# Kernel optimization log

Measured on AMD Instinct MI355X. Metric: run time of the kernel, lower is better.

Reference implementation:

```python
import jax, jax.numpy as jnp
import numpy as np

DT = 0.1
TAU_HP = 12.3  # Tm1 high-pass time constant
TAU_LP = 2.3   # Tm1 low-pass time constant

N_NEURONS = 200_000
N_EDGES = 6_400_000
N_TM1 = 25_000
STEPS = 50


def setup_inputs() -> dict:
    key = jax.random.key(0)
    k1, k2, k3, k4 = jax.random.split(key, 4)
    tm1_input = jax.random.normal(k1, (STEPS, N_TM1), dtype=jnp.float32)
    weights = jax.random.normal(k2, (N_EDGES,), dtype=jnp.float32) * 0.1
    tau = jnp.ones((N_NEURONS,), dtype=jnp.float32)      # tau_init = 1.0 per type
    vrest = jnp.zeros((N_NEURONS,), dtype=jnp.float32)   # vrest_init = 0.0 per type
    source_idx = jax.random.randint(k3, (N_EDGES,), 0, N_NEURONS, dtype=jnp.int32)
    target_idx = jax.random.randint(k4, (N_EDGES,), 0, N_NEURONS, dtype=jnp.int32)
    return {
        "tm1_input": tm1_input,
        "weights": weights,
        "tau": tau,
        "vrest": vrest,
        "source_idx": source_idx,
        "target_idx": target_idx,
        "n_tm1": N_TM1,
    }


def reference(tm1_input, weights, tau, vrest, source_idx, target_idx, n_tm1):
    n_neurons = tau.shape[0]

    def step(carry, x):
        v, tm1_f, tm1_v = carry
        # Tm1 temporal filters: high-pass then rectify then low-pass
        hp_out = x - tm1_f                                   # [n_tm1]
        tm1_f_new = tm1_f + DT * (x - tm1_f) / TAU_HP
        rect_out = jax.nn.relu(hp_out)
        # write (old) tm1_v into the Tm1 slice of v before recurrence
        v = v.at[:n_tm1].set(tm1_v)
        tm1_v_new = tm1_v + DT * (rect_out - tm1_v) / TAU_LP
        # gather -> weight -> scatter-add message passing
        r = jax.nn.relu(v)                                   # [n_neurons]
        edge_currents = r[source_idx] * weights              # [n_edges]
        synaptic_input = jax.ops.segment_sum(
            edge_currents, target_idx, num_segments=n_neurons)
        external = jnp.zeros_like(v).at[:n_tm1].set(tm1_v_new)
        dv = (-v + synaptic_input + vrest + external) / tau
        dv = dv.at[:n_tm1].set(0.0)                          # Tm1 driven by its filters
        v = v + DT * dv
        return (v, tm1_f_new, tm1_v_new), None

    v0 = jnp.zeros((tau.shape[0],), dtype=tm1_input.dtype)
    f0 = jnp.zeros((n_tm1,), dtype=tm1_input.dtype)
    tv0 = jnp.zeros((n_tm1,), dtype=tm1_input.dtype)
    (v, _, _), _ = jax.lax.scan(step, (v0, f0, tv0), tm1_input)
    return v[None, :]  # [1, n_neurons], matches torch batch=1
```

## Files before the change

### kernel.cpp

```cpp
#include <hip/hip_runtime.h>
#include <hip/hip_bf16.h>

#define DT 0.1f
#define TAU_HP 12.3f
#define TAU_LP 2.3f
#define SCAN_B 1024

#define BSHIFT 7
#define BMASK 127
#define BMAX 2048
#define CHUNK 16384
#define B4_CAP 6144


__global__ void init_kernel(float* __restrict__ v,
                            float* __restrict__ tm1_f,
                            float* __restrict__ tm1_v,
                            int n_neurons, int n_tm1) {
    int i = blockIdx.x * blockDim.x + threadIdx.x;
    if (i < n_neurons) v[i] = 0.0f;
    if (i < n_tm1) { tm1_f[i] = 0.0f; tm1_v[i] = 0.0f; }
}

__global__ void bhist_kernel(const int* __restrict__ tgt, int* __restrict__ blkhist,
                             int n_edges, int nb, int nblk) {
    __shared__ int hist[BMAX];
    int b = blockIdx.x;
    for (int i = threadIdx.x; i < nb; i += blockDim.x) hist[i] = 0;
    __syncthreads();
    int base = b * CHUNK;
    int end = min(base + CHUNK, n_edges);
    for (int k = base + threadIdx.x; k < end; k += blockDim.x)
        atomicAdd(&hist[tgt[k] >> BSHIFT], 1);
    __syncthreads();
    for (int i = threadIdx.x; i < nb; i += blockDim.x)
        blkhist[(size_t)i * nblk + b] = hist[i];
}

__global__ void scan1_kernel(const int* in, int* out, int* bsums, int n) {
    __shared__ int s[SCAN_B];
    int gid = blockIdx.x * SCAN_B + threadIdx.x;
    int x = (gid < n) ? in[gid] : 0;
    s[threadIdx.x] = x;
    __syncthreads();
    for (int off = 1; off < SCAN_B; off <<= 1) {
        int t = (threadIdx.x >= off) ? s[threadIdx.x - off] : 0;
        __syncthreads();
        s[threadIdx.x] += t;
        __syncthreads();
    }
    if (gid < n) out[gid] = s[threadIdx.x] - x;
    if (threadIdx.x == SCAN_B - 1) bsums[blockIdx.x] = s[SCAN_B - 1];
}

__global__ void scan2_kernel(int* bsums, int nb) {
    __shared__ int s[SCAN_B];
    int x = (threadIdx.x < nb) ? bsums[threadIdx.x] : 0;
    s[threadIdx.x] = x;
    __syncthreads();
    for (int off = 1; off < SCAN_B; off <<= 1) {
        int t = (threadIdx.x >= off) ? s[threadIdx.x - off] : 0;
        __syncthreads();
        s[threadIdx.x] += t;
        __syncthreads();
    }
    if (threadIdx.x < nb) bsums[threadIdx.x] = s[threadIdx.x] - x;
}

__global__ void scanadd_kernel(int* data, const int* __restrict__ bsums, int n) {
    int gid = blockIdx.x * blockDim.x + threadIdx.x;
    if (gid < n) data[gid] += bsums[gid / SCAN_B];
}

__global__ void bin_kernel(const int* __restrict__ src, const int* __restrict__ tgt,
                           const float* __restrict__ w, const int* __restrict__ scanned,
                           int2* __restrict__ edges, int n_edges, int nb, int nblk) {
    __shared__ int cur[BMAX];
    int b = blockIdx.x;
    for (int i = threadIdx.x; i < nb; i += blockDim.x)
        cur[i] = scanned[(size_t)i * nblk + b];
    __syncthreads();
    int base = b * CHUNK;
    int end = min(base + CHUNK, n_edges);
    for (int k = base + threadIdx.x; k < end; k += blockDim.x) {
        int t = tgt[k];
        int pos = atomicAdd(&cur[t >> BSHIFT], 1);
        edges[pos] = make_int2(src[k] | ((t & BMASK) << 18), __float_as_int(w[k]));
    }
}

__global__ void finalize_kernel(int2* edges, const int* __restrict__ scanned,
                                int* __restrict__ row_start,
                                int n_neurons, int n_edges, int nb, int nblk) {
    __shared__ int2 buf[B4_CAP];
    __shared__ int hist[BMASK + 1], ls[BMASK + 1], cur[BMASK + 1];
    int b = blockIdx.x;
    int beg = scanned[(size_t)b * nblk];
    int end = (b == nb - 1) ? n_edges : scanned[(size_t)(b + 1) * nblk];
    int n = min(end - beg, B4_CAP);

    for (int k = threadIdx.x; k < n; k += blockDim.x) buf[k] = edges[beg + k];
    if (threadIdx.x <= BMASK) hist[threadIdx.x] = 0;
    __syncthreads();
    for (int k = threadIdx.x; k < n; k += blockDim.x)
        atomicAdd(&hist[(buf[k].x >> 18) & BMASK], 1);
    __syncthreads();
    if (threadIdx.x <= BMASK) ls[threadIdx.x] = hist[threadIdx.x];
    __syncthreads();
    for (int off = 1; off <= BMASK; off <<= 1) {
        int t = (threadIdx.x <= BMASK && threadIdx.x >= off) ? ls[threadIdx.x - off] : 0;
        __syncthreads();
        if (threadIdx.x <= BMASK) ls[threadIdx.x] += t;
        __syncthreads();
    }
    if (threadIdx.x <= BMASK) {
        int excl = ls[threadIdx.x] - hist[threadIdx.x];
        cur[threadIdx.x] = excl;
        int t = (b << BSHIFT) + threadIdx.x;
        if (t < n_neurons) row_start[t] = beg + excl;
    }
    if (b == nb - 1 && threadIdx.x == 0) row_start[n_neurons] = n_edges;
    __syncthreads();
    for (int k = threadIdx.x; k < n; k += blockDim.x) {
        int2 r = buf[k];
        int pos = atomicAdd(&cur[(r.x >> 18) & BMASK], 1);
        edges[beg + pos] = make_int2(r.x & 0x3FFFF, r.y);
    }
}


__global__ void neuron_kernel(float* __restrict__ v,
                              const float* __restrict__ syn,
                              float* __restrict__ tm1_f,
                              float* __restrict__ tm1_v,
                              const float* __restrict__ x,
                              const float* __restrict__ tau,
                              const float* __restrict__ vrest,
                              int n_neurons, int n_tm1, int do_update) {
    int i = blockIdx.x * blockDim.x + threadIdx.x;
    if (i >= n_neurons) return;

    if (i < n_tm1) {
        float f  = tm1_f[i];
        float tv = tm1_v[i];
        float xi = x[i];
        float hp = xi - f;
        tm1_f[i] = f + DT * (xi - f) / TAU_HP;
        v[i] = tv;
        float rect = fmaxf(hp, 0.0f);
        tm1_v[i] = tv + DT * (rect - tv) / TAU_LP;
    } else if (do_update) {
        float vi = v[i];
        float dv = (-vi + syn[i] + vrest[i]) / tau[i];
        v[i] = vi + DT * dv;
    }
}

__global__ void gather_kernel(const int* __restrict__ row_start,
                              const int2* __restrict__ edges,
                              const float* __restrict__ v,
                              float* __restrict__ syn, int n) {
    int tid  = blockIdx.x * blockDim.x + threadIdx.x;
    int row  = tid >> 4;
    int lane = tid & 15;
    if (row >= n) return;
    int s = row_start[row];
    int e = row_start[row + 1];
    float sum = 0.0f;
    for (int p = (s & ~1) + 2 * lane; p < e; p += 32) {
        int4 q = *(const int4*)(edges + p);
        if (p >= s)     sum += fmaxf(v[q.x], 0.0f) * __int_as_float(q.y);
        if (p + 1 < e)  sum += fmaxf(v[q.z], 0.0f) * __int_as_float(q.w);
    }
    sum += __shfl_xor(sum, 8);
    sum += __shfl_xor(sum, 4);
    sum += __shfl_xor(sum, 2);
    sum += __shfl_xor(sum, 1);
    if (lane == 0) syn[row] = sum;
}

__global__ void final_kernel(const float* __restrict__ v,
                             const float* __restrict__ syn,
                             const float* __restrict__ tau,
                             const float* __restrict__ vrest,
                             float* __restrict__ out,
                             int n_neurons, int n_tm1) {
    int i = blockIdx.x * blockDim.x + threadIdx.x;
    if (i >= n_neurons) return;
    float vi = v[i];
    if (i >= n_tm1) {
        vi = vi + DT * ((-vi + syn[i] + vrest[i]) / tau[i]);
    }
    out[i] = vi;
}

extern "C" void kernel_launch(void* const* d_in, const int* in_sizes, int n_in,
                              void* d_out, int out_size, void* d_ws, size_t ws_size,
                              hipStream_t stream) {
    const float* tm1_input  = (const float*)d_in[0];
    const float* weights    = (const float*)d_in[1];
    const float* tau        = (const float*)d_in[2];
    const float* vrest      = (const float*)d_in[3];
    const int*   source_idx = (const int*)d_in[4];
    const int*   target_idx = (const int*)d_in[5];

    const int n_edges   = in_sizes[1];
    const int n_neurons = in_sizes[2];
    const int n_tm1     = 25000;
    const int steps     = in_sizes[0] / n_tm1;

    const int nb   = (n_neurons + BMASK) >> BSHIFT;
    const int nblk = (n_edges + CHUNK - 1) / CHUNK;
    const int n_scan = nb * nblk;

    size_t off = 0;
    auto alloc = [&](size_t n) { size_t o = off; off += n; return o; };
    int* ws_i = (int*)d_ws;
    float* ws_f = (float*)d_ws;

    int2*  edges     = (int2*)(ws_i + alloc((size_t)(n_edges + 2) * 2));
    float* v         = ws_f + alloc(n_neurons);
    float* syn       = ws_f + alloc(n_neurons);
    float* tm1_f     = ws_f + alloc(n_tm1);
    float* tm1_v     = ws_f + alloc(n_tm1);
    int*   row_start = ws_i + alloc(n_neurons + 1);
    int*   blkhist   = ws_i + alloc((size_t)n_scan);
    int*   bsums     = ws_i + alloc(SCAN_B);
    (void)ws_size;

    float* out = (float*)d_out;

    const int B = 256;
    const int gridN = (n_neurons + B - 1) / B;
    const int gridG = ((n_neurons * 16) + B - 1) / B;
    const int nScanBlocks = (n_scan + SCAN_B - 1) / SCAN_B;
    const int gridSA = (n_scan + B - 1) / B;

    init_kernel<<<gridN, B, 0, stream>>>(v, tm1_f, tm1_v, n_neurons, n_tm1);
    bhist_kernel<<<nblk, 1024, 0, stream>>>(target_idx, blkhist, n_edges, nb, nblk);
    scan1_kernel<<<nScanBlocks, SCAN_B, 0, stream>>>(blkhist, blkhist, bsums, n_scan);
    scan2_kernel<<<1, SCAN_B, 0, stream>>>(bsums, nScanBlocks);
    scanadd_kernel<<<gridSA, B, 0, stream>>>(blkhist, bsums, n_scan);
    bin_kernel<<<nblk, 1024, 0, stream>>>(source_idx, target_idx, weights, blkhist,
                                          edges, n_edges, nb, nblk);
    finalize_kernel<<<nb, 1024, 0, stream>>>(edges, blkhist, row_start,
                                             n_neurons, n_edges, nb, nblk);

    for (int t = 0; t < steps; ++t) {
        neuron_kernel<<<gridN, B, 0, stream>>>(
            v, syn, tm1_f, tm1_v,
            tm1_input + (size_t)t * n_tm1,
            tau, vrest, n_neurons, n_tm1, t > 0 ? 1 : 0);
        gather_kernel<<<gridG, B, 0, stream>>>(row_start, edges, v, syn, n_neurons);
    }

    final_kernel<<<gridN, B, 0, stream>>>(v, syn, tau, vrest, out, n_neurons, n_tm1);
}
```

Baseline: 2.149 ms.

## Fuse neuron update into gather with ping-pong state and drop Tm1-target edges

Merges the per-step neuron update and the synaptic gather into one step kernel that reads the previous state buffer and writes the next, double-buffering v. This removes the separate update kernel, the syn array round trip and the final kernel. Edges whose target is a Tm1 neuron are dropped while the CSR is built, since their synaptic input is overwritten anyway, which shrinks the per-step gather. The Tm1 low-pass state is now carried in v itself, and the binning chunk size is doubled. The risk is in the restructured Tm1 recurrence and last-step handling, which must still match the reference.

```diff
diff --git a/kernel.cpp b/kernel.cpp
--- a/kernel.cpp
+++ b/kernel.cpp
@@ -9,29 +9,30 @@
 #define BSHIFT 7
 #define BMASK 127
 #define BMAX 2048
-#define CHUNK 16384
+#define CHUNK 32768
 #define B4_CAP 6144
 
 
-__global__ void init_kernel(float* __restrict__ v,
+__global__ void init_kernel(float* __restrict__ vA,
                             float* __restrict__ tm1_f,
-                            float* __restrict__ tm1_v,
                             int n_neurons, int n_tm1) {
     int i = blockIdx.x * blockDim.x + threadIdx.x;
-    if (i < n_neurons) v[i] = 0.0f;
-    if (i < n_tm1) { tm1_f[i] = 0.0f; tm1_v[i] = 0.0f; }
+    if (i < n_neurons) vA[i] = 0.0f;
+    if (i < n_tm1) tm1_f[i] = 0.0f;
 }
 
 __global__ void bhist_kernel(const int* __restrict__ tgt, int* __restrict__ blkhist,
-                             int n_edges, int nb, int nblk) {
+                             int n_edges, int n_tm1, int nb, int nblk) {
     __shared__ int hist[BMAX];
     int b = blockIdx.x;
     for (int i = threadIdx.x; i < nb; i += blockDim.x) hist[i] = 0;
     __syncthreads();
     int base = b * CHUNK;
     int end = min(base + CHUNK, n_edges);
-    for (int k = base + threadIdx.x; k < end; k += blockDim.x)
-        atomicAdd(&hist[tgt[k] >> BSHIFT], 1);
+    for (int k = base + threadIdx.x; k < end; k += blockDim.x) {
+        int t = tgt[k];
+        if (t >= n_tm1) atomicAdd(&hist[t >> BSHIFT], 1);
+    }
     __syncthreads();
     for (int i = threadIdx.x; i < nb; i += blockDim.x)
         blkhist[(size_t)i * nblk + b] = hist[i];
@@ -53,7 +54,7 @@
     if (threadIdx.x == SCAN_B - 1) bsums[blockIdx.x] = s[SCAN_B - 1];
 }
 
-__global__ void scan2_kernel(int* bsums, int nb) {
+__global__ void scan2_kernel(int* bsums, int nb, int* total) {
     __shared__ int s[SCAN_B];
     int x = (threadIdx.x < nb) ? bsums[threadIdx.x] : 0;
     s[threadIdx.x] = x;
@@ -64,6 +65,7 @@
         s[threadIdx.x] += t;
         __syncthreads();
     }
+    if (threadIdx.x == nb - 1) *total = s[threadIdx.x];
     if (threadIdx.x < nb) bsums[threadIdx.x] = s[threadIdx.x] - x;
 }
 
@@ -74,7 +76,8 @@
 
 __global__ void bin_kernel(const int* __restrict__ src, const int* __restrict__ tgt,
                            const float* __restrict__ w, const int* __restrict__ scanned,
-                           int2* __restrict__ edges, int n_edges, int nb, int nblk) {
+                           int2* __restrict__ edges, int n_edges, int n_tm1,
+                           int nb, int nblk) {
     __shared__ int cur[BMAX];
     int b = blockIdx.x;
     for (int i = threadIdx.x; i < nb; i += blockDim.x)
@@ -84,6 +87,7 @@
     int end = min(base + CHUNK, n_edges);
     for (int k = base + threadIdx.x; k < end; k += blockDim.x) {
         int t = tgt[k];
+        if (t < n_tm1) continue;
         int pos = atomicAdd(&cur[t >> BSHIFT], 1);
         edges[pos] = make_int2(src[k] | ((t & BMASK) << 18), __float_as_int(w[k]));
     }
@@ -91,12 +95,14 @@
 
 __global__ void finalize_kernel(int2* edges, const int* __restrict__ scanned,
                                 int* __restrict__ row_start,
-                                int n_neurons, int n_edges, int nb, int nblk) {
+                                const int* __restrict__ total,
+                                int n_neurons, int nb, int nblk) {
     __shared__ int2 buf[B4_CAP];
     __shared__ int hist[BMASK + 1], ls[BMASK + 1], cur[BMASK + 1];
     int b = blockIdx.x;
+    int n_kept = *total;
     int beg = scanned[(size_t)b * nblk];
-    int end = (b == nb - 1) ? n_edges : scanned[(size_t)(b + 1) * nblk];
+    int end = (b == nb - 1) ? n_kept : scanned[(size_t)(b + 1) * nblk];
     int n = min(end - beg, B4_CAP);
 
     for (int k = threadIdx.x; k < n; k += blockDim.x) buf[k] = edges[beg + k];
@@ -119,7 +125,7 @@
         int t = (b << BSHIFT) + threadIdx.x;
         if (t < n_neurons) row_start[t] = beg + excl;
     }
-    if (b == nb - 1 && threadIdx.x == 0) row_start[n_neurons] = n_edges;
+    if (b == nb - 1 && threadIdx.x == 0) row_start[n_neurons] = n_kept;
     __syncthreads();
     for (int k = threadIdx.x; k < n; k += blockDim.x) {
         int2 r = buf[k];
@@ -128,70 +134,52 @@
     }
 }
 
-
-__global__ void neuron_kernel(float* __restrict__ v,
-                              const float* __restrict__ syn,
-                              float* __restrict__ tm1_f,
-                              float* __restrict__ tm1_v,
-                              const float* __restrict__ x,
-                              const float* __restrict__ tau,
-                              const float* __restrict__ vrest,
-                              int n_neurons, int n_tm1, int do_update) {
-    int i = blockIdx.x * blockDim.x + threadIdx.x;
-    if (i >= n_neurons) return;
-
-    if (i < n_tm1) {
-        float f  = tm1_f[i];
-        float tv = tm1_v[i];
-        float xi = x[i];
-        float hp = xi - f;
-        tm1_f[i] = f + DT * (xi - f) / TAU_HP;
-        v[i] = tv;
-        float rect = fmaxf(hp, 0.0f);
-        tm1_v[i] = tv + DT * (rect - tv) / TAU_LP;
-    } else if (do_update) {
-        float vi = v[i];
-        float dv = (-vi + syn[i] + vrest[i]) / tau[i];
-        v[i] = vi + DT * dv;
-    }
-}
-
-__global__ void gather_kernel(const int* __restrict__ row_start,
-                              const int2* __restrict__ edges,
-                              const float* __restrict__ v,
-                              float* __restrict__ syn, int n) {
+__global__ void step_kernel(const int* __restrict__ row_start,
+                            const int2* __restrict__ edges,
+                            const float* __restrict__ vr,
+                            float* __restrict__ vw,
+                            float* __restrict__ tm1_f,
+                            const float* __restrict__ x,
+                            const float* __restrict__ tau,
+                            const float* __restrict__ vrest,
+                            int n_neurons, int n_tm1, int last) {
     int tid  = blockIdx.x * blockDim.x + threadIdx.x;
     int row  = tid >> 4;
     int lane = tid & 15;
-    if (row >= n) return;
+    if (row >= n_neurons) return;
+
+    if (row < n_tm1) {
+        if (lane == 0) {
+            float cur = vr[row];
+            if (last) {
+                vw[row] = cur;
+            } else {
+                float f  = tm1_f[row];
+                float xk = x[row];
+                float hp = xk - f;
+                tm1_f[row] = f + DT * (xk - f) / TAU_HP;
+                vw[row] = cur + DT * (fmaxf(hp, 0.0f) - cur) / TAU_LP;
+            }
+        }
+        return;
+    }
+
     int s = row_start[row];
     int e = row_start[row + 1];
     float sum = 0.0f;
     for (int p = (s & ~1) + 2 * lane; p < e; p += 32) {
         int4 q = *(const int4*)(edges + p);
-        if (p >= s)     sum += fmaxf(v[q.x], 0.0f) * __int_as_float(q.y);
-        if (p + 1 < e)  sum += fmaxf(v[q.z], 0.0f) * __int_as_float(q.w);
+        if (p >= s)    sum += fmaxf(vr[q.x], 0.0f) * __int_as_float(q.y);
+        if (p + 1 < e) sum += fmaxf(vr[q.z], 0.0f) * __int_as_float(q.w);
     }
     sum += __shfl_xor(sum, 8);
     sum += __shfl_xor(sum, 4);
     sum += __shfl_xor(sum, 2);
     sum += __shfl_xor(sum, 1);
-    if (lane == 0) syn[row] = sum;
-}
-
-__global__ void final_kernel(const float* __restrict__ v,
-                             const float* __restrict__ syn,
-                             const float* __restrict__ tau,
-                             const float* __restrict__ vrest,
-                             float* __restrict__ out,
-                             int n_neurons, int n_tm1) {
-    int i = blockIdx.x * blockDim.x + threadIdx.x;
-    if (i >= n_neurons) return;
-    float vi = v[i];
-    if (i >= n_tm1) {
-        vi = vi + DT * ((-vi + syn[i] + vrest[i]) / tau[i]);
-    }
-    out[i] = vi;
+    if (lane == 0) {
+        float vi = vr[row];
+        vw[row] = vi + DT * ((-vi + sum + vrest[row]) / tau[row]);
+    }
 }
 
 extern "C" void kernel_launch(void* const* d_in, const int* in_sizes, int n_in,
@@ -219,13 +207,13 @@
     float* ws_f = (float*)d_ws;
 
     int2*  edges     = (int2*)(ws_i + alloc((size_t)(n_edges + 2) * 2));
-    float* v         = ws_f + alloc(n_neurons);
-    float* syn       = ws_f + alloc(n_neurons);
+    float* vA        = ws_f + alloc(n_neurons);
+    float* vB        = ws_f + alloc(n_neurons);
     float* tm1_f     = ws_f + alloc(n_tm1);
-    float* tm1_v     = ws_f + alloc(n_tm1);
     int*   row_start = ws_i + alloc(n_neurons + 1);
     int*   blkhist   = ws_i + alloc((size_t)n_scan);
     int*   bsums     = ws_i + alloc(SCAN_B);
+    int*   total     = ws_i + alloc(1);
     (void)ws_size;
 
     float* out = (float*)d_out;
@@ -236,23 +224,23 @@
     const int nScanBlocks = (n_scan + SCAN_B - 1) / SCAN_B;
     const int gridSA = (n_scan + B - 1) / B;
 
-    init_kernel<<<gridN, B, 0, stream>>>(v, tm1_f, tm1_v, n_neurons, n_tm1);
-    bhist_kernel<<<nblk, 1024, 0, stream>>>(target_idx, blkhist, n_edges, nb, nblk);
+    init_kernel<<<gridN, B, 0, stream>>>(vA, tm1_f, n_neurons, n_tm1);
+    bhist_kernel<<<nblk, 1024, 0, stream>>>(target_idx, blkhist, n_edges, n_tm1,
+                                            nb, nblk);
     scan1_kernel<<<nScanBlocks, SCAN_B, 0, stream>>>(blkhist, blkhist, bsums, n_scan);
-    scan2_kernel<<<1, SCAN_B, 0, stream>>>(bsums, nScanBlocks);
+    scan2_kernel<<<1, SCAN_B, 0, stream>>>(bsums, nScanBlocks, total);
     scanadd_kernel<<<gridSA, B, 0, stream>>>(blkhist, bsums, n_scan);
     bin_kernel<<<nblk, 1024, 0, stream>>>(source_idx, target_idx, weights, blkhist,
-                                          edges, n_edges, nb, nblk);
-    finalize_kernel<<<nb, 1024, 0, stream>>>(edges, blkhist, row_start,
-                                             n_neurons, n_edges, nb, nblk);
-
-    for (int t = 0; t < steps; ++t) {
-        neuron_kernel<<<gridN, B, 0, stream>>>(
-            v, syn, tm1_f, tm1_v,
-            tm1_input + (size_t)t * n_tm1,
-            tau, vrest, n_neurons, n_tm1, t > 0 ? 1 : 0);
-        gather_kernel<<<gridG, B, 0, stream>>>(row_start, edges, v, syn, n_neurons);
-    }
-
-    final_kernel<<<gridN, B, 0, stream>>>(v, syn, tau, vrest, out, n_neurons, n_tm1);
-}
+                                          edges, n_edges, n_tm1, nb, nblk);
+    finalize_kernel<<<nb, 1024, 0, stream>>>(edges, blkhist, row_start, total,
+                                             n_neurons, nb, nblk);
+
+    for (int k = 0; k < steps; ++k) {
+        const float* vr = (k & 1) ? vB : vA;
+        float* vw = (k == steps - 1) ? out : ((k & 1) ? vA : vB);
+        step_kernel<<<gridG, B, 0, stream>>>(
+            row_start, edges, vr, vw, tm1_f,
+            tm1_input + (size_t)k * n_tm1,
+            tau, vrest, n_neurons, n_tm1, (k == steps - 1) ? 1 : 0);
+    }
+}
```

New measurement: 1.836 ms. 14.6% less time.
